# Optimization experiments

Measured on AMD Instinct MI355X. Metric: run time of the kernel, lower is better.

## Reference

```python
import jax, jax.numpy as jnp
import numpy as np

PAD = 0

def setup_inputs() -> dict:
    key = jax.random.key(0)
    k1, k2, k3, k4 = jax.random.split(key, 4)
    B, S, F, V, H, D = 64, 256, 4, 50257, 768, 512
    words = jax.random.randint(k1, (B, S, F), 0, V, dtype=jnp.int64)  # pad_index=0 occurs rarely at random
    E = jax.random.normal(k2, (V, H), dtype=jnp.float32) * 0.02      # stand-in for transformer last_hidden_state producer
    W = jax.random.normal(k3, (H, D), dtype=jnp.float32) * 0.02      # FFN projection weight
    b = jax.random.normal(k4, (D,), dtype=jnp.float32) * 0.02
    return {"words": words, "E": E, "W": W, "b": b}

def reference(words, E, W, b):
    # words: [B, S, F] subword ids; mask out pad subwords
    mask = (words != PAD)                                  # [B,S,F] bool
    sub = E[words] * mask[..., None].astype(E.dtype)       # [B,S,F,H], pads zeroed
    cnt = mask.sum(-1).astype(E.dtype)                     # [B,S] subwords per word
    # segment-mean over the fix_len axis; fully-padded words -> 0 (matches pad_sequence(..., 0))
    word_emb = sub.sum(-2) / jnp.maximum(cnt, 1.0)[..., None]   # [B,S,H]
    word_emb = jnp.where((cnt > 0)[..., None], word_emb, 0.0)
    return word_emb @ W + b                                # [B,S,D]
```

## Files before the change

### kernel.cpp

```cpp
#include <hip/hip_runtime.h>
#include <hip/hip_bf16.h>

#define M_TOT 16384
#define K_TOT 768
#define N_TOT 512
#define BM 64
#define NT (K_TOT / 64)

typedef __attribute__((ext_vector_type(8))) __bf16 bf16x8;
typedef __attribute__((ext_vector_type(4))) float f32x4;

static __device__ __forceinline__ ushort f2bf(float x) {
  union { float f; unsigned int u; } v; v.f = x;
  unsigned int r = v.u + 0x7fffu + ((v.u >> 16) & 1u);
  return (ushort)(r >> 16);
}
static __device__ __forceinline__ unsigned pack2(float lo, float hi) {
  return (unsigned)f2bf(lo) | ((unsigned)f2bf(hi) << 16);
}

static __device__ __forceinline__ void load_lds16(const ushort* g, ushort* l) {
  __builtin_amdgcn_global_load_lds(
      (const __attribute__((address_space(1))) void*)g,
      (__attribute__((address_space(3))) void*)l, 16, 0, 0);
}

__global__ __launch_bounds__(256) void wt_kernel(const float* __restrict__ W,
                                                 ushort* __restrict__ Wt) {
  __shared__ float tile[64][65];
  const int t  = threadIdx.x;
  const int k0 = blockIdx.x * 64;
  const int n0 = blockIdx.y * 64;
#pragma unroll
  for (int i = 0; i < 4; ++i) {
    const int idx = t + i * 256;
    const int r = idx >> 4;
    const int c = (idx & 15) * 4;
    const float4 v =
        *reinterpret_cast<const float4*>(W + (size_t)(k0 + r) * N_TOT + n0 + c);
    tile[r][c + 0] = v.x; tile[r][c + 1] = v.y;
    tile[r][c + 2] = v.z; tile[r][c + 3] = v.w;
  }
  __syncthreads();
#pragma unroll
  for (int i = 0; i < 4; ++i) {
    const int idx = t + i * 256;
    const int rn = idx >> 4;
    const int ck = (idx & 15) * 4;
    ushort4 o;
    o.x = f2bf(tile[ck + 0][rn]);
    o.y = f2bf(tile[ck + 1][rn]);
    o.z = f2bf(tile[ck + 2][rn]);
    o.w = f2bf(tile[ck + 3][rn]);
    *reinterpret_cast<ushort4*>(Wt + (size_t)(n0 + rn) * K_TOT + k0 + ck) = o;
  }
}

__global__ __launch_bounds__(512, 2) void fused_kernel(
    const int* __restrict__ words, const float* __restrict__ E,
    const ushort* __restrict__ Bt, const float* __restrict__ bias,
    float* __restrict__ out) {
  __shared__ ushort Bl[2][N_TOT * 64];
  __shared__ ushort Al[2][BM * 64];
  __shared__ int   eoff_l[BM][4];
  __shared__ float msk_l[BM][4];
  __shared__ float scl_l[BM];

  const int t    = threadIdx.x;
  const int lane = t & 63;
  const int w    = t >> 6;
  const int wr   = w >> 2;
  const int wc   = w & 3;
  const int bm   = blockIdx.x;

  if (t < BM) {
    const int4 w4 =
        *reinterpret_cast<const int4*>(words + (size_t)(bm * BM + t) * 4);
    const int ids[4] = {w4.x, w4.y, w4.z, w4.w};
    float cnt = 0.f;
#pragma unroll
    for (int f = 0; f < 4; ++f) {
      eoff_l[t][f] = ids[f] * K_TOT;
      const float m = (ids[f] != 0) ? 1.f : 0.f;
      msk_l[t][f] = m;
      cnt += m;
    }
    scl_l[t] = (cnt > 0.f) ? (1.f / cnt) : 0.f;
  }
  __syncthreads();

  const int sr = t >> 3;
  const int ss = t & 7;
  const float4* pf[4];
#pragma unroll
  for (int f = 0; f < 4; ++f)
    pf[f] = reinterpret_cast<const float4*>(E + eoff_l[sr][f] + ss * 8);
  const float m0 = msk_l[sr][0], m1 = msk_l[sr][1];
  const float m2 = msk_l[sr][2], m3 = msk_l[sr][3];
  const float scl = scl_l[sr];
  const ushort* bB = Bt + (size_t)sr * K_TOT + ss * 8;

  f32x4 acc[2][8];
#pragma unroll
  for (int m = 0; m < 2; ++m)
#pragma unroll
    for (int n = 0; n < 8; ++n) acc[m][n] = (f32x4){0.f, 0.f, 0.f, 0.f};

  float4 va[8];

#define A_LOAD(kt)                                                           \
  do {                                                                       \
    _Pragma("unroll") for (int f = 0; f < 4; ++f) {                          \
      va[2 * f + 0] = pf[f][(kt) * 16 + 0];                                  \
      va[2 * f + 1] = pf[f][(kt) * 16 + 1];                                  \
    }                                                                        \
  } while (0)

#define STAGE_B(dst, kt)                                                     \
  do {                                                                       \
    _Pragma("unroll") for (int i = 0; i < 8; ++i) {                          \
      load_lds16(bB + (size_t)i * 64 * K_TOT + (kt) * 64,                    \
                 &(dst)[(i * 512 + w * 64) * 8]);                            \
    }                                                                        \
  } while (0)

#define A_MATH(dst)                                                          \
  do {                                                                       \
    float s[8];                                                              \
    _Pragma("unroll") for (int j = 0; j < 4; ++j) {                          \
      s[j] = (va[0][j] * m0 + va[2][j] * m1 + va[4][j] * m2 + va[6][j] * m3) \
             * scl;                                                          \
      s[4 + j] =                                                             \
          (va[1][j] * m0 + va[3][j] * m1 + va[5][j] * m2 + va[7][j] * m3) *  \
          scl;                                                               \
    }                                                                        \
    uint4 o;                                                                 \
    o.x = pack2(s[0], s[1]); o.y = pack2(s[2], s[3]);                        \
    o.z = pack2(s[4], s[5]); o.w = pack2(s[6], s[7]);                        \
    *reinterpret_cast<uint4*>(&(dst)[sr * 64 + ss * 8]) = o;                 \
  } while (0)

#define COMPUTE(Ar, Br)                                                      \
  do {                                                                       \
    _Pragma("unroll") for (int kk = 0; kk < 2; ++kk) {                       \
      const int ks = kk * 4 + (lane >> 4);                                   \
      bf16x8 af[2], bfr[8];                                                  \
      _Pragma("unroll") for (int m = 0; m < 2; ++m)                          \
        af[m] = *reinterpret_cast<const bf16x8*>(                            \
            &(Ar)[(wr * 32 + m * 16 + (lane & 15)) * 64 + ks * 8]);          \
      _Pragma("unroll") for (int n = 0; n < 8; ++n)                          \
        bfr[n] = *reinterpret_cast<const bf16x8*>(                           \
            &(Br)[(wc * 128 + n * 16 + (lane & 15)) * 64 + ks * 8]);         \
      __builtin_amdgcn_s_setprio(1);                                         \
      _Pragma("unroll") for (int m = 0; m < 2; ++m)                          \
        _Pragma("unroll") for (int n = 0; n < 8; ++n)                        \
          acc[m][n] = __builtin_amdgcn_mfma_f32_16x16x32_bf16(               \
              af[m], bfr[n], acc[m][n], 0, 0, 0);                            \
      __builtin_amdgcn_s_setprio(0);                                         \
    }                                                                        \
  } while (0)

  A_LOAD(0);
  STAGE_B(Bl[0], 0);
  A_MATH(Al[0]);
  __syncthreads();

  int cur = 0;
  for (int kt = 0; kt < NT; ++kt) {
    const ushort* Ar = cur ? Al[1] : Al[0];
    const ushort* Br = cur ? Bl[1] : Bl[0];
    ushort* An = cur ? Al[0] : Al[1];
    ushort* Bn = cur ? Bl[0] : Bl[1];
    if (kt + 1 < NT) {
      A_LOAD(kt + 1);
      STAGE_B(Bn, kt + 1);
    }
    COMPUTE(Ar, Br);
    if (kt + 1 < NT) A_MATH(An);
    __syncthreads();
    cur ^= 1;
  }
#undef A_LOAD
#undef STAGE_B
#undef A_MATH
#undef COMPUTE

  const int col  = wc * 128 + (lane & 15);
  const int row0 = bm * BM + wr * 32 + ((lane >> 4) << 2);
#pragma unroll
  for (int n = 0; n < 8; ++n) {
    const float bv = bias[col + n * 16];
#pragma unroll
    for (int m = 0; m < 2; ++m) {
#pragma unroll
      for (int j = 0; j < 4; ++j) {
        __builtin_nontemporal_store(
            acc[m][n][j] + bv,
            &out[(size_t)(row0 + m * 16 + j) * N_TOT + col + n * 16]);
      }
    }
  }
}

extern "C" void kernel_launch(void* const* d_in, const int* in_sizes, int n_in,
                              void* d_out, int out_size, void* d_ws,
                              size_t ws_size, hipStream_t stream) {
  const int*   words = (const int*)d_in[0];
  const float* E     = (const float*)d_in[1];
  const float* W     = (const float*)d_in[2];
  const float* b     = (const float*)d_in[3];
  float* out = (float*)d_out;

  ushort* Wtws = (ushort*)d_ws;

  hipLaunchKernelGGL(wt_kernel, dim3(K_TOT / 64, N_TOT / 64), dim3(256), 0,
                     stream, W, Wtws);
  hipLaunchKernelGGL(fused_kernel, dim3(M_TOT / BM), dim3(512), 0, stream,
                     words, E, Wtws, b, out);
}
```

Before: 63.99 us.

## Gather full A tile into swizzled LDS, read W fragments directly from global

Restructures the fused gather+GEMM. Each block handles 32 rows and first gathers, averages and stores the whole 32x768 bf16 A tile into XOR-swizzled LDS. It then runs the MFMA loop reading B fragments straight from a pre-chunked bf16 W layout in global memory/L2, with no LDS staging or per-step barriers. This removes the double-buffered B LDS traffic and the sync per k-step, and shrinks LDS use to allow more resident blocks. In exchange the gather and the compute no longer overlap, and W is re-read from L2 by twice as many blocks.

Result: faster. 54.46 us (-14.9%).

```diff
diff --git a/kernel.cpp b/kernel.cpp
--- a/kernel.cpp
+++ b/kernel.cpp
@@ -4,8 +4,9 @@
 #define M_TOT 16384
 #define K_TOT 768
 #define N_TOT 512
-#define BM 64
-#define NT (K_TOT / 64)
+#define BM 32
+#define NT 12
+#define NSLOT 96
 
 typedef __attribute__((ext_vector_type(8))) __bf16 bf16x8;
 typedef __attribute__((ext_vector_type(4))) float f32x4;
@@ -17,12 +18,6 @@
 }
 static __device__ __forceinline__ unsigned pack2(float lo, float hi) {
   return (unsigned)f2bf(lo) | ((unsigned)f2bf(hi) << 16);
-}
-
-static __device__ __forceinline__ void load_lds16(const ushort* g, ushort* l) {
-  __builtin_amdgcn_global_load_lds(
-      (const __attribute__((address_space(1))) void*)g,
-      (__attribute__((address_space(3))) void*)l, 16, 0, 0);
 }
 
 __global__ __launch_bounds__(256) void wt_kernel(const float* __restrict__ W,
@@ -52,16 +47,19 @@
     o.y = f2bf(tile[ck + 1][rn]);
     o.z = f2bf(tile[ck + 2][rn]);
     o.w = f2bf(tile[ck + 3][rn]);
-    *reinterpret_cast<ushort4*>(Wt + (size_t)(n0 + rn) * K_TOT + k0 + ck) = o;
-  }
-}
-
-__global__ __launch_bounds__(512, 2) void fused_kernel(
+    const int kg    = k0 + ck;
+    const int chunk = kg >> 3;
+    const int e0    = kg & 7;
+    *reinterpret_cast<ushort4*>(
+        &Wt[((size_t)chunk * N_TOT + n0 + rn) * 8 + e0]) = o;
+  }
+}
+
+__global__ __launch_bounds__(256, 2) void fused_kernel(
     const int* __restrict__ words, const float* __restrict__ E,
-    const ushort* __restrict__ Bt, const float* __restrict__ bias,
+    const ushort* __restrict__ Wt, const float* __restrict__ bias,
     float* __restrict__ out) {
-  __shared__ ushort Bl[2][N_TOT * 64];
-  __shared__ ushort Al[2][BM * 64];
+  __shared__ ushort A_l[BM * NSLOT * 8];
   __shared__ int   eoff_l[BM][4];
   __shared__ float msk_l[BM][4];
   __shared__ float scl_l[BM];
@@ -69,8 +67,6 @@
   const int t    = threadIdx.x;
   const int lane = t & 63;
   const int w    = t >> 6;
-  const int wr   = w >> 2;
-  const int wc   = w & 3;
   const int bm   = blockIdx.x;
 
   if (t < BM) {
@@ -91,6 +87,7 @@
 
   const int sr = t >> 3;
   const int ss = t & 7;
+  const int sw = ss ^ (sr & 7);
   const float4* pf[4];
 #pragma unroll
   for (int f = 0; f < 4; ++f)
@@ -98,17 +95,8 @@
   const float m0 = msk_l[sr][0], m1 = msk_l[sr][1];
   const float m2 = msk_l[sr][2], m3 = msk_l[sr][3];
   const float scl = scl_l[sr];
-  const ushort* bB = Bt + (size_t)sr * K_TOT + ss * 8;
-
-  f32x4 acc[2][8];
-#pragma unroll
-  for (int m = 0; m < 2; ++m)
-#pragma unroll
-    for (int n = 0; n < 8; ++n) acc[m][n] = (f32x4){0.f, 0.f, 0.f, 0.f};
-
-  float4 va[8];
-
-#define A_LOAD(kt)                                                           \
+
+#define A_LOAD(va, kt)                                                       \
   do {                                                                       \
     _Pragma("unroll") for (int f = 0; f < 4; ++f) {                          \
       va[2 * f + 0] = pf[f][(kt) * 16 + 0];                                  \
@@ -116,15 +104,7 @@
     }                                                                        \
   } while (0)
 
-#define STAGE_B(dst, kt)                                                     \
-  do {                                                                       \
-    _Pragma("unroll") for (int i = 0; i < 8; ++i) {                          \
-      load_lds16(bB + (size_t)i * 64 * K_TOT + (kt) * 64,                    \
-                 &(dst)[(i * 512 + w * 64) * 8]);                            \
-    }                                                                        \
-  } while (0)
-
-#define A_MATH(dst)                                                          \
+#define A_MATH(va, kt)                                                       \
   do {                                                                       \
     float s[8];                                                              \
     _Pragma("unroll") for (int j = 0; j < 4; ++j) {                          \
@@ -137,66 +117,72 @@
     uint4 o;                                                                 \
     o.x = pack2(s[0], s[1]); o.y = pack2(s[2], s[3]);                        \
     o.z = pack2(s[4], s[5]); o.w = pack2(s[6], s[7]);                        \
-    *reinterpret_cast<uint4*>(&(dst)[sr * 64 + ss * 8]) = o;                 \
+    *reinterpret_cast<uint4*>(&A_l[((sr) * NSLOT + (kt) * 8 + sw) * 8]) = o; \
   } while (0)
 
-#define COMPUTE(Ar, Br)                                                      \
-  do {                                                                       \
-    _Pragma("unroll") for (int kk = 0; kk < 2; ++kk) {                       \
-      const int ks = kk * 4 + (lane >> 4);                                   \
-      bf16x8 af[2], bfr[8];                                                  \
-      _Pragma("unroll") for (int m = 0; m < 2; ++m)                          \
-        af[m] = *reinterpret_cast<const bf16x8*>(                            \
-            &(Ar)[(wr * 32 + m * 16 + (lane & 15)) * 64 + ks * 8]);          \
-      _Pragma("unroll") for (int n = 0; n < 8; ++n)                          \
-        bfr[n] = *reinterpret_cast<const bf16x8*>(                           \
-            &(Br)[(wc * 128 + n * 16 + (lane & 15)) * 64 + ks * 8]);         \
-      __builtin_amdgcn_s_setprio(1);                                         \
-      _Pragma("unroll") for (int m = 0; m < 2; ++m)                          \
-        _Pragma("unroll") for (int n = 0; n < 8; ++n)                        \
-          acc[m][n] = __builtin_amdgcn_mfma_f32_16x16x32_bf16(               \
-              af[m], bfr[n], acc[m][n], 0, 0, 0);                            \
-      __builtin_amdgcn_s_setprio(0);                                         \
-    }                                                                        \
-  } while (0)
-
-  A_LOAD(0);
-  STAGE_B(Bl[0], 0);
-  A_MATH(Al[0]);
+  {
+    float4 vaA[8], vaB[8];
+    A_LOAD(vaA, 0);
+    A_LOAD(vaB, 1);
+#pragma unroll
+    for (int kt = 0; kt < NT; kt += 2) {
+      A_MATH(vaA, kt);
+      if (kt + 2 < NT) A_LOAD(vaA, kt + 2);
+      A_MATH(vaB, kt + 1);
+      if (kt + 3 < NT) A_LOAD(vaB, kt + 3);
+    }
+  }
+#undef A_LOAD
+#undef A_MATH
   __syncthreads();
 
-  int cur = 0;
+  f32x4 acc[2][8];
+#pragma unroll
+  for (int m = 0; m < 2; ++m)
+#pragma unroll
+    for (int n = 0; n < 8; ++n) acc[m][n] = (f32x4){0.f, 0.f, 0.f, 0.f};
+
+  const int colBase = w * 128 + (lane & 15);
+  const int rsel    = lane & 15;
+  const int ksel    = lane >> 4;
+
+#pragma unroll 2
   for (int kt = 0; kt < NT; ++kt) {
-    const ushort* Ar = cur ? Al[1] : Al[0];
-    const ushort* Br = cur ? Bl[1] : Bl[0];
-    ushort* An = cur ? Al[0] : Al[1];
-    ushort* Bn = cur ? Bl[0] : Bl[1];
-    if (kt + 1 < NT) {
-      A_LOAD(kt + 1);
-      STAGE_B(Bn, kt + 1);
-    }
-    COMPUTE(Ar, Br);
-    if (kt + 1 < NT) A_MATH(An);
-    __syncthreads();
-    cur ^= 1;
-  }
-#undef A_LOAD
-#undef STAGE_B
-#undef A_MATH
-#undef COMPUTE
-
-  const int col  = wc * 128 + (lane & 15);
-  const int row0 = bm * BM + wr * 32 + ((lane >> 4) << 2);
+#pragma unroll
+    for (int kk = 0; kk < 2; ++kk) {
+      const int ks = kk * 4 + ksel;
+      bf16x8 af[2], bfr[8];
+#pragma unroll
+      for (int m = 0; m < 2; ++m) {
+        const int row = m * 16 + rsel;
+        af[m] = *reinterpret_cast<const bf16x8*>(
+            &A_l[(row * NSLOT + kt * 8 + (ks ^ (row & 7))) * 8]);
+      }
+#pragma unroll
+      for (int n = 0; n < 8; ++n) {
+        bfr[n] = *reinterpret_cast<const bf16x8*>(
+            &Wt[((size_t)(kt * 8 + ks) * N_TOT + colBase + n * 16) * 8]);
+      }
+#pragma unroll
+      for (int m = 0; m < 2; ++m)
+#pragma unroll
+        for (int n = 0; n < 8; ++n)
+          acc[m][n] = __builtin_amdgcn_mfma_f32_16x16x32_bf16(
+              af[m], bfr[n], acc[m][n], 0, 0, 0);
+    }
+  }
+
+  const int row0 = bm * BM + (ksel << 2);
 #pragma unroll
   for (int n = 0; n < 8; ++n) {
-    const float bv = bias[col + n * 16];
+    const float bv = bias[colBase + n * 16];
 #pragma unroll
     for (int m = 0; m < 2; ++m) {
 #pragma unroll
       for (int j = 0; j < 4; ++j) {
         __builtin_nontemporal_store(
             acc[m][n][j] + bv,
-            &out[(size_t)(row0 + m * 16 + j) * N_TOT + col + n * 16]);
+            &out[(size_t)(row0 + m * 16 + j) * N_TOT + colBase + n * 16]);
       }
     }
   }
@@ -215,6 +201,6 @@
 
   hipLaunchKernelGGL(wt_kernel, dim3(K_TOT / 64, N_TOT / 64), dim3(256), 0,
                      stream, W, Wtws);
-  hipLaunchKernelGGL(fused_kernel, dim3(M_TOT / BM), dim3(512), 0, stream,
+  hipLaunchKernelGGL(fused_kernel, dim3(M_TOT / BM), dim3(256), 0, stream,
                      words, E, Wtws, b, out);
 }
```
